# Kernel optimization log

Measured on AMD Instinct MI355X. Metric: run time of the kernel, lower is better.

Reference implementation:

```python
import jax, jax.numpy as jnp
import numpy as np

EMBED = 1024
HEADS = 16
HEAD_DIM = EMBED // HEADS


def setup_inputs() -> dict:
    key = jax.random.key(0)
    ks = jax.random.split(key, 7)
    B, Sd, Se = 4, 2048, 2048
    dec = jax.random.normal(ks[0], (B, Sd, EMBED), dtype=jnp.float32)
    enc = jax.random.normal(ks[1], (B, Se, EMBED), dtype=jnp.float32)
    scale = 1.0 / np.sqrt(EMBED)
    W_q = jax.random.normal(ks[2], (EMBED, EMBED), dtype=jnp.float32) * scale
    W_k = jax.random.normal(ks[3], (EMBED, EMBED), dtype=jnp.float32) * scale
    W_v = jax.random.normal(ks[4], (EMBED, EMBED), dtype=jnp.float32) * scale
    W_o = jax.random.normal(ks[5], (EMBED, EMBED), dtype=jnp.float32) * scale
    b_o = jax.random.normal(ks[6], (EMBED,), dtype=jnp.float32) * 0.01
    return {"decoder_input": dec, "encoder_output": enc,
            "W_q": W_q, "W_k": W_k, "W_v": W_v, "W_o": W_o, "b_o": b_o}


def reference(decoder_input, encoder_output, W_q, W_k, W_v, W_o, b_o):
    B, Sd, E = decoder_input.shape
    Se = encoder_output.shape[1]
    # projections (nn.Linear applies x @ W.T; here W is stored as [in, out])
    Q = (decoder_input @ W_q).reshape(B, Sd, HEADS, HEAD_DIM)
    K = (encoder_output @ W_k).reshape(B, Se, HEADS, HEAD_DIM)
    V = (encoder_output @ W_v).reshape(B, Se, HEADS, HEAD_DIM)
    # scores: [B, H, Sd, Se]
    scores = jnp.einsum('bqhd,bkhd->bhqk', Q, K) / jnp.sqrt(jnp.float32(HEAD_DIM))
    attn = jax.nn.softmax(scores, axis=-1)
    out = jnp.einsum('bhqk,bkhd->bqhd', attn, V).reshape(B, Sd, E)
    return out @ W_o + b_o
```

## Files before the change

kernel.cpp:

```cpp
#include <hip/hip_runtime.h>
#include <hip/hip_bf16.h>

namespace {

typedef __attribute__((ext_vector_type(8))) short bf16x8;
typedef __attribute__((ext_vector_type(4))) float f32x4;
typedef __attribute__((ext_vector_type(4))) unsigned u32x4v;

constexpr int BATCH = 4;
constexpr int SEQ   = 2048;
constexpr int EMB   = 1024;
constexpr int NH    = 16;
constexpr int HD    = 64;
constexpr int MTOT  = BATCH * SEQ;
constexpr float LOG2E = 1.44269504088896f;
constexpr float SOFTMAX_C = 16.0f;

__device__ __forceinline__ unsigned short f2bf(float x) {
    unsigned int u = __float_as_uint(x);
    u += 0x7fffu + ((u >> 16) & 1u);
    return (unsigned short)(u >> 16);
}

__device__ __forceinline__ void gl_lds16(const void* g, void* l) {
    __builtin_amdgcn_global_load_lds(
        (const __attribute__((address_space(1))) unsigned int*)g,
        (__attribute__((address_space(3))) unsigned int*)l, 16, 0, 0);
}

__global__ __launch_bounds__(256)
void prep(const float* __restrict__ dec, const float* __restrict__ enc,
          unsigned short* __restrict__ decb, unsigned short* __restrict__ encb,
          const float* __restrict__ W0, const float* __restrict__ W1,
          const float* __restrict__ W2, const float* __restrict__ W3,
          unsigned short* __restrict__ WtBase, float qscale)
{
    __shared__ __align__(16) unsigned short Ts[64][65];
    const int tid = threadIdx.x;
    const int bid = blockIdx.x;
    if (bid < 16384) {
        const int zz = bid >> 13;
        const int i = (bid & 8191) * 256 + tid;
        const float* src = zz ? enc : dec;
        unsigned short* dst = zz ? encb : decb;
        float4 v = ((const float4*)src)[i];
        ushort4 o;
        o.x = f2bf(v.x); o.y = f2bf(v.y); o.z = f2bf(v.z); o.w = f2bf(v.w);
        ((ushort4*)dst)[i] = o;
        return;
    }
    const int zid = bid - 16384;
    const int z = zid >> 8;
    const float* W = (z == 0) ? W0 : (z == 1) ? W1 : (z == 2) ? W2 : W3;
    unsigned short* Wt = WtBase + (size_t)z * EMB * EMB;
    const float scale = (z == 0) ? qscale : 1.0f;
    const int n0 = (zid & 15) * 64, k0 = ((zid >> 4) & 15) * 64;
    #pragma unroll
    for (int i = 0; i < 4; ++i) {
        int id = tid + i * 256;
        int r = id >> 4, q = id & 15;
        float4 v = *(const float4*)&W[(size_t)(k0 + r) * EMB + n0 + q * 4];
        Ts[q * 4 + 0][r] = f2bf(v.x * scale);
        Ts[q * 4 + 1][r] = f2bf(v.y * scale);
        Ts[q * 4 + 2][r] = f2bf(v.z * scale);
        Ts[q * 4 + 3][r] = f2bf(v.w * scale);
    }
    __syncthreads();
    #pragma unroll
    for (int i = 0; i < 4; ++i) {
        int id = tid + i * 256;
        int rn = id >> 4, q = id & 15;
        ushort4 o;
        o.x = Ts[rn][q * 4 + 0]; o.y = Ts[rn][q * 4 + 1];
        o.z = Ts[rn][q * 4 + 2]; o.w = Ts[rn][q * 4 + 3];
        *(ushort4*)&Wt[(size_t)(n0 + rn) * EMB + k0 + q * 4] = o;
    }
}

enum OutKind { OUT_BF16R, OUT_F32B, OUT_VTK };

template<int OK>
__device__ __forceinline__
void gemm_body(unsigned short* lds,
               const unsigned short* __restrict__ A, const unsigned short* __restrict__ Bt,
               const float* __restrict__ bias, void* __restrict__ Cout,
               int m0, int n0, int N, int Kd)
{
    const int tid  = threadIdx.x;
    const int lane = tid & 63, wave = tid >> 6;
    const int g = lane >> 4, c = lane & 15;
    const int wm = (wave & 1) * 64, wn = (wave >> 1) * 64;

    const int r0 = tid >> 2, s = tid & 3;
    const int sg = s ^ ((r0 + (r0 >> 2)) & 3);
    const unsigned short* ga0 = A  + (size_t)(m0 + r0)      * Kd + sg * 8;
    const unsigned short* ga1 = A  + (size_t)(m0 + r0 + 64) * Kd + sg * 8;
    const unsigned short* gb0 = Bt + (size_t)(n0 + r0)      * Kd + sg * 8;
    const unsigned short* gb1 = Bt + (size_t)(n0 + r0 + 64) * Kd + sg * 8;
    const int lo0 = tid * 8, lo1 = (256 + tid) * 8;

    const int cs = (c + (c >> 2)) & 3;

    f32x4 acc[4][4];
    #pragma unroll
    for (int i = 0; i < 4; ++i)
        #pragma unroll
        for (int j = 0; j < 4; ++j) acc[i][j] = (f32x4)0.0f;

    gl_lds16(ga0, &lds[lo0]);        gl_lds16(ga1, &lds[lo1]);
    gl_lds16(gb0, &lds[8192 + lo0]); gl_lds16(gb1, &lds[8192 + lo1]);
    ga0 += 32; ga1 += 32; gb0 += 32; gb1 += 32;
    __syncthreads();

    const int KT = Kd / 32;
    for (int kt = 0; kt < KT; kt += 2) {
        #pragma unroll
        for (int h2 = 0; h2 < 2; ++h2) {
            const int k = kt + h2;
            const int bcur = h2 * 4096, bnxt = (h2 ^ 1) * 4096;
            if (k + 1 < KT) {
                gl_lds16(ga0, &lds[bnxt + lo0]);        gl_lds16(ga1, &lds[bnxt + lo1]);
                gl_lds16(gb0, &lds[8192 + bnxt + lo0]); gl_lds16(gb1, &lds[8192 + bnxt + lo1]);
                ga0 += 32; ga1 += 32; gb0 += 32; gb1 += 32;
            }
            bf16x8 af[4], bfr[4];
            #pragma unroll
            for (int mt = 0; mt < 4; ++mt)
                af[mt]  = *(const bf16x8*)&lds[bcur + (wm + mt * 16 + c) * 32 + (g ^ cs) * 8];
            #pragma unroll
            for (int nt = 0; nt < 4; ++nt)
                bfr[nt] = *(const bf16x8*)&lds[8192 + bcur + (wn + nt * 16 + c) * 32 + (g ^ cs) * 8];
            #pragma unroll
            for (int mt = 0; mt < 4; ++mt)
                #pragma unroll
                for (int nt = 0; nt < 4; ++nt) {
                    if (OK == OUT_VTK)
                        acc[mt][nt] = __builtin_amdgcn_mfma_f32_16x16x32_bf16(af[mt], bfr[nt], acc[mt][nt], 0, 0, 0);
                    else
                        acc[mt][nt] = __builtin_amdgcn_mfma_f32_16x16x32_bf16(bfr[nt], af[mt], acc[mt][nt], 0, 0, 0);
                }
            __syncthreads();
        }
    }

    if (OK == OUT_VTK) {
        unsigned short* Vt = (unsigned short*)Cout;
        #pragma unroll
        for (int mt = 0; mt < 4; ++mt) {
            int m  = m0 + wm + mt * 16 + 4 * g;
            int bb = m >> 11, sl = m & 2047;
            int sp = (sl & ~31) | (((sl >> 2) & 3) << 3) | (((sl >> 4) & 1) << 2);
            #pragma unroll
            for (int nt = 0; nt < 4; ++nt) {
                int np = n0 + wn + nt * 16 + c;
                ushort4 o;
                o.x = f2bf(acc[mt][nt][0]); o.y = f2bf(acc[mt][nt][1]);
                o.z = f2bf(acc[mt][nt][2]); o.w = f2bf(acc[mt][nt][3]);
                *(ushort4*)&Vt[((size_t)bb * 1024 + np) * SEQ + sp] = o;
            }
        }
        return;
    }

    if (OK == OUT_BF16R) {
        unsigned short* C = (unsigned short*)Cout;
        #pragma unroll
        for (int mt = 0; mt < 4; ++mt) {
            int m = m0 + wm + mt * 16 + c;
            #pragma unroll
            for (int nt = 0; nt < 4; ++nt) {
                int n = n0 + wn + nt * 16 + 4 * g;
                unsigned u0, u1;
                asm("v_cvt_pk_bf16_f32 %0, %1, %2" : "=v"(u0) : "v"(acc[mt][nt][0]), "v"(acc[mt][nt][1]));
                asm("v_cvt_pk_bf16_f32 %0, %1, %2" : "=v"(u1) : "v"(acc[mt][nt][2]), "v"(acc[mt][nt][3]));
                uint2 st; st.x = u0; st.y = u1;
                *(uint2*)&C[(size_t)m * N + n] = st;
            }
        }
        return;
    }

    {
        float* C = (float*)Cout;
        #pragma unroll
        for (int nt = 0; nt < 4; ++nt) {
            int n = n0 + wn + nt * 16 + 4 * g;
            float4 bv = *(const float4*)&bias[n];
            #pragma unroll
            for (int mt = 0; mt < 4; ++mt) {
                int m = m0 + wm + mt * 16 + c;
                float4 o;
                o.x = acc[mt][nt][0] + bv.x;
                o.y = acc[mt][nt][1] + bv.y;
                o.z = acc[mt][nt][2] + bv.z;
                o.w = acc[mt][nt][3] + bv.w;
                *(float4*)&C[(size_t)m * N + n] = o;
            }
        }
    }
}

__global__ __launch_bounds__(256)
void proj_fused(const unsigned short* __restrict__ decb, const unsigned short* __restrict__ encb,
                const unsigned short* __restrict__ WtBase,
                unsigned short* __restrict__ Qb, unsigned short* __restrict__ Kb,
                unsigned short* __restrict__ Vtg)
{
    __shared__ __align__(16) unsigned short lds[16384];
    const int fid = blockIdx.y * 24 + blockIdx.x;
    const int xcd = fid & 7, idx = fid >> 3;
    const int mt  = (xcd << 3) | (idx / 24);
    const int nt  = idx % 24;
    const int m0  = mt * 128;
    const size_t SML = (size_t)EMB * EMB;
    if (nt < 8) {
        gemm_body<OUT_BF16R>(lds, decb, WtBase, nullptr, Qb, m0, nt * 128, EMB, EMB);
    } else if (nt < 16) {
        gemm_body<OUT_BF16R>(lds, encb, WtBase + SML, nullptr, Kb,
                             m0, (nt - 8) * 128, EMB, EMB);
    } else {
        gemm_body<OUT_VTK>(lds, encb, WtBase + 2 * SML, nullptr, Vtg,
                           m0, (nt - 16) * 128, 0, EMB);
    }
}

__global__ __launch_bounds__(256)
void proj_out(const unsigned short* __restrict__ Ob, const unsigned short* __restrict__ WoT,
              const float* __restrict__ bo, float* __restrict__ out)
{
    __shared__ __align__(16) unsigned short lds[16384];
    const int fid = blockIdx.y * 8 + blockIdx.x;
    const int xcd = fid & 7, idx = fid >> 3;
    const int mt  = (xcd << 3) | (idx >> 3);
    const int nt  = idx & 7;
    gemm_body<OUT_F32B>(lds, Ob, WoT, bo, out, mt * 128, nt * 128, EMB, EMB);
}

__global__ __launch_bounds__(256)
void attn(const unsigned short* __restrict__ Q, const unsigned short* __restrict__ K,
          const unsigned short* __restrict__ Vt, unsigned short* __restrict__ O)
{
    __shared__ __align__(16) unsigned short Ks[2][64 * 64];
    __shared__ __align__(16) unsigned short Vs[2][64 * 64];

    const int tid  = threadIdx.x;
    const int lane = tid & 63, wave = tid >> 6;
    const int g = lane >> 4, c = lane & 15, c7 = c & 7;

    const int fid  = blockIdx.y * 32 + blockIdx.x;
    const int xcd  = fid & 7, idx = fid >> 3;
    const int bh   = (xcd << 3) | (idx >> 5);
    const int qblk = idx & 31;
    const int b = bh >> 4, h = bh & 15;
    const int qw = qblk * 64 + wave * 16;

    const unsigned short* Qp0 = Q + (size_t)(b * SEQ + qw + c) * EMB + h * HD;
    bf16x8 qb[2];
    qb[0] = *(const bf16x8*)(Qp0 + g * 8);
    qb[1] = *(const bf16x8*)(Qp0 + 32 + g * 8);

    const int r0 = tid >> 3, s8 = tid & 7;
    const int sg = s8 ^ (r0 & 7);
    const unsigned short* gK0 = K + ((size_t)b * SEQ + r0) * EMB + h * HD + sg * 8;
    const unsigned short* gK1 = gK0 + (size_t)32 * EMB;
    const unsigned short* gV0 = Vt + (size_t)bh * HD * SEQ + (size_t)r0 * SEQ + sg * 8;
    const unsigned short* gV1 = gV0 + (size_t)32 * SEQ;
    const int lo0 = tid * 8, lo1 = (256 + tid) * 8;

    f32x4 oac[4];
    #pragma unroll
    for (int dt = 0; dt < 4; ++dt) oac[dt] = (f32x4)0.0f;
    f32x4 lacc = (f32x4)0.0f;
    const f32x4 minit = {-SOFTMAX_C, -SOFTMAX_C, -SOFTMAX_C, -SOFTMAX_C};
    const short onebf = (short)0x3F80;
    const bf16x8 vones = {onebf, onebf, onebf, onebf, onebf, onebf, onebf, onebf};

    gl_lds16(gK0, &Ks[0][lo0]); gl_lds16(gK1, &Ks[0][lo1]);
    gl_lds16(gV0, &Vs[0][lo0]); gl_lds16(gV1, &Vs[0][lo1]);
    gK0 += (size_t)64 * EMB; gK1 += (size_t)64 * EMB; gV0 += 64; gV1 += 64;
    __syncthreads();

    constexpr int T = SEQ / 64;
    for (int t = 0; t < T; t += 2) {
        #pragma unroll
        for (int h2 = 0; h2 < 2; ++h2) {
            const int tt = t + h2;
            if (tt + 1 < T) {
                gl_lds16(gK0, &Ks[h2 ^ 1][lo0]); gl_lds16(gK1, &Ks[h2 ^ 1][lo1]);
                gl_lds16(gV0, &Vs[h2 ^ 1][lo0]); gl_lds16(gV1, &Vs[h2 ^ 1][lo1]);
                gK0 += (size_t)64 * EMB; gK1 += (size_t)64 * EMB;
                gV0 += 64;               gV1 += 64;
            }

            f32x4 st[4];
            __builtin_amdgcn_s_setprio(1);
            #pragma unroll
            for (int kt = 0; kt < 4; ++kt) {
                bf16x8 ka0 = *(const bf16x8*)&Ks[h2][(kt * 16 + c) * 64 + (g ^ c7) * 8];
                bf16x8 ka1 = *(const bf16x8*)&Ks[h2][(kt * 16 + c) * 64 + ((4 + g) ^ c7) * 8];
                st[kt] = __builtin_amdgcn_mfma_f32_16x16x32_bf16(ka0, qb[0], minit, 0, 0, 0);
                st[kt] = __builtin_amdgcn_mfma_f32_16x16x32_bf16(ka1, qb[1], st[kt], 0, 0, 0);
            }
            __builtin_amdgcn_s_setprio(0);

            bf16x8 pa[2];
            {
                unsigned uu[8];
                #pragma unroll
                for (int kt = 0; kt < 4; ++kt) {
                    float p0 = __builtin_amdgcn_exp2f(st[kt][0]);
                    float p1 = __builtin_amdgcn_exp2f(st[kt][1]);
                    float p2 = __builtin_amdgcn_exp2f(st[kt][2]);
                    float p3 = __builtin_amdgcn_exp2f(st[kt][3]);
                    asm("v_cvt_pk_bf16_f32 %0, %1, %2" : "=v"(uu[2 * kt])     : "v"(p0), "v"(p1));
                    asm("v_cvt_pk_bf16_f32 %0, %1, %2" : "=v"(uu[2 * kt + 1]) : "v"(p2), "v"(p3));
                }
                u32x4v w0 = {uu[0], uu[1], uu[2], uu[3]};
                u32x4v w1 = {uu[4], uu[5], uu[6], uu[7]};
                pa[0] = __builtin_bit_cast(bf16x8, w0);
                pa[1] = __builtin_bit_cast(bf16x8, w1);
            }

            __builtin_amdgcn_s_setprio(1);
            #pragma unroll
            for (int dt = 0; dt < 4; ++dt) {
                bf16x8 vb0 = *(const bf16x8*)&Vs[h2][(dt * 16 + c) * 64 + (g ^ c7) * 8];
                bf16x8 vb1 = *(const bf16x8*)&Vs[h2][(dt * 16 + c) * 64 + ((4 + g) ^ c7) * 8];
                oac[dt] = __builtin_amdgcn_mfma_f32_16x16x32_bf16(pa[0], vb0, oac[dt], 0, 0, 0);
                oac[dt] = __builtin_amdgcn_mfma_f32_16x16x32_bf16(pa[1], vb1, oac[dt], 0, 0, 0);
            }
            lacc = __builtin_amdgcn_mfma_f32_16x16x32_bf16(pa[0], vones, lacc, 0, 0, 0);
            lacc = __builtin_amdgcn_mfma_f32_16x16x32_bf16(pa[1], vones, lacc, 0, 0, 0);
            __builtin_amdgcn_s_setprio(0);

            __syncthreads();
        }
    }

    unsigned short* Op = O + (size_t)(b * SEQ + qw) * EMB + h * HD;
    #pragma unroll
    for (int r = 0; r < 4; ++r) {
        float linv = 1.0f / lacc[r];
        #pragma unroll
        for (int dt = 0; dt < 4; ++dt)
            Op[(size_t)(4 * g + r) * EMB + dt * 16 + c] = f2bf(oac[dt][r] * linv);
    }
}

}

extern "C" void kernel_launch(void* const* d_in, const int* in_sizes, int n_in,
                              void* d_out, int out_size, void* d_ws, size_t ws_size,
                              hipStream_t stream)
{
    const float* dec = (const float*)d_in[0];
    const float* enc = (const float*)d_in[1];
    const float* Wq  = (const float*)d_in[2];
    const float* Wk  = (const float*)d_in[3];
    const float* Wv  = (const float*)d_in[4];
    const float* Wo  = (const float*)d_in[5];
    const float* bo  = (const float*)d_in[6];
    float* out = (float*)d_out;

    const size_t BIG = (size_t)MTOT * EMB;
    const size_t SML = (size_t)EMB * EMB;
    unsigned short* decb = (unsigned short*)d_ws;
    unsigned short* encb = decb + BIG;
    unsigned short* WqT  = encb + BIG;
    unsigned short* WoT  = WqT + 3 * SML;
    unsigned short* Qb   = WqT + 4 * SML;
    unsigned short* Kb   = Qb + BIG;
    unsigned short* Vtg  = Kb + BIG;
    unsigned short* Ob   = Vtg + BIG;

    dim3 blk(256);

    prep<<<dim3(16384 + 1024), blk, 0, stream>>>(
        dec, enc, decb, encb, Wq, Wk, Wv, Wo, WqT, 0.125f * LOG2E);

    proj_fused<<<dim3(24, MTOT / 128), blk, 0, stream>>>(decb, encb, WqT, Qb, Kb, Vtg);

    attn<<<dim3(SEQ / 64, BATCH * NH), blk, 0, stream>>>(Qb, Kb, Vtg, Ob);

    proj_out<<<dim3(EMB / 128, MTOT / 128), blk, 0, stream>>>(Ob, WoT, bo, out);
}
```

Baseline: 302.3 us.

## Halve attention KV tile to raise occupancy and reorder GEMM tile mapping

The attention kernel now streams K/V in 32-key tiles instead of 64, which halves LDS use, and requests 8 blocks per CU through launch bounds so more waves can hide latency. Each iteration therefore does half the MFMA work, with twice as many barriers and loop trips. The projection GEMMs also change their block-to-tile mapping so that consecutive blocks on an XCD share the N tile (weights) across M tiles, aiming at better L2 reuse. Risks are the extra synchronization overhead per key and possible register pressure from the occupancy bound.

Measured after the change: 325.7 us. 7.8% more time.

```diff
diff --git a/kernel.cpp b/kernel.cpp
--- a/kernel.cpp
+++ b/kernel.cpp
@@ -209,8 +209,8 @@
     __shared__ __align__(16) unsigned short lds[16384];
     const int fid = blockIdx.y * 24 + blockIdx.x;
     const int xcd = fid & 7, idx = fid >> 3;
-    const int mt  = (xcd << 3) | (idx / 24);
-    const int nt  = idx % 24;
+    const int nt  = idx >> 3;
+    const int mt  = (xcd << 3) | (idx & 7);
     const int m0  = mt * 128;
     const size_t SML = (size_t)EMB * EMB;
     if (nt < 8) {
@@ -231,21 +231,21 @@
     __shared__ __align__(16) unsigned short lds[16384];
     const int fid = blockIdx.y * 8 + blockIdx.x;
     const int xcd = fid & 7, idx = fid >> 3;
-    const int mt  = (xcd << 3) | (idx >> 3);
-    const int nt  = idx & 7;
+    const int nt  = idx >> 3;
+    const int mt  = (xcd << 3) | (idx & 7);
     gemm_body<OUT_F32B>(lds, Ob, WoT, bo, out, mt * 128, nt * 128, EMB, EMB);
 }
 
-__global__ __launch_bounds__(256)
+__global__ __launch_bounds__(256, 8)
 void attn(const unsigned short* __restrict__ Q, const unsigned short* __restrict__ K,
           const unsigned short* __restrict__ Vt, unsigned short* __restrict__ O)
 {
-    __shared__ __align__(16) unsigned short Ks[2][64 * 64];
-    __shared__ __align__(16) unsigned short Vs[2][64 * 64];
+    __shared__ __align__(16) unsigned short Ks[2][32 * 64];
+    __shared__ __align__(16) unsigned short Vs[2][64 * 32];
 
     const int tid  = threadIdx.x;
     const int lane = tid & 63, wave = tid >> 6;
-    const int g = lane >> 4, c = lane & 15, c7 = c & 7;
+    const int g = lane >> 4, c = lane & 15, c7 = c & 7, c3 = c & 3;
 
     const int fid  = blockIdx.y * 32 + blockIdx.x;
     const int xcd  = fid & 7, idx = fid >> 3;
@@ -259,13 +259,13 @@
     qb[0] = *(const bf16x8*)(Qp0 + g * 8);
     qb[1] = *(const bf16x8*)(Qp0 + 32 + g * 8);
 
-    const int r0 = tid >> 3, s8 = tid & 7;
-    const int sg = s8 ^ (r0 & 7);
-    const unsigned short* gK0 = K + ((size_t)b * SEQ + r0) * EMB + h * HD + sg * 8;
-    const unsigned short* gK1 = gK0 + (size_t)32 * EMB;
-    const unsigned short* gV0 = Vt + (size_t)bh * HD * SEQ + (size_t)r0 * SEQ + sg * 8;
-    const unsigned short* gV1 = gV0 + (size_t)32 * SEQ;
-    const int lo0 = tid * 8, lo1 = (256 + tid) * 8;
+    const int r0k = tid >> 3, s8 = tid & 7;
+    const int sgk = s8 ^ (r0k & 7);
+    const unsigned short* gK = K + ((size_t)b * SEQ + r0k) * EMB + h * HD + sgk * 8;
+    const int r0v = tid >> 2, s4 = tid & 3;
+    const int sgv = s4 ^ (r0v & 3);
+    const unsigned short* gV = Vt + ((size_t)bh * HD + r0v) * SEQ + sgv * 8;
+    const int lo = tid * 8;
 
     f32x4 oac[4];
     #pragma unroll
@@ -275,27 +275,24 @@
     const short onebf = (short)0x3F80;
     const bf16x8 vones = {onebf, onebf, onebf, onebf, onebf, onebf, onebf, onebf};
 
-    gl_lds16(gK0, &Ks[0][lo0]); gl_lds16(gK1, &Ks[0][lo1]);
-    gl_lds16(gV0, &Vs[0][lo0]); gl_lds16(gV1, &Vs[0][lo1]);
-    gK0 += (size_t)64 * EMB; gK1 += (size_t)64 * EMB; gV0 += 64; gV1 += 64;
+    gl_lds16(gK, &Ks[0][lo]); gl_lds16(gV, &Vs[0][lo]);
+    gK += (size_t)32 * EMB; gV += 32;
     __syncthreads();
 
-    constexpr int T = SEQ / 64;
+    constexpr int T = SEQ / 32;
     for (int t = 0; t < T; t += 2) {
         #pragma unroll
         for (int h2 = 0; h2 < 2; ++h2) {
             const int tt = t + h2;
             if (tt + 1 < T) {
-                gl_lds16(gK0, &Ks[h2 ^ 1][lo0]); gl_lds16(gK1, &Ks[h2 ^ 1][lo1]);
-                gl_lds16(gV0, &Vs[h2 ^ 1][lo0]); gl_lds16(gV1, &Vs[h2 ^ 1][lo1]);
-                gK0 += (size_t)64 * EMB; gK1 += (size_t)64 * EMB;
-                gV0 += 64;               gV1 += 64;
-            }
-
-            f32x4 st[4];
+                gl_lds16(gK, &Ks[h2 ^ 1][lo]); gl_lds16(gV, &Vs[h2 ^ 1][lo]);
+                gK += (size_t)32 * EMB; gV += 32;
+            }
+
+            f32x4 st[2];
             __builtin_amdgcn_s_setprio(1);
             #pragma unroll
-            for (int kt = 0; kt < 4; ++kt) {
+            for (int kt = 0; kt < 2; ++kt) {
                 bf16x8 ka0 = *(const bf16x8*)&Ks[h2][(kt * 16 + c) * 64 + (g ^ c7) * 8];
                 bf16x8 ka1 = *(const bf16x8*)&Ks[h2][(kt * 16 + c) * 64 + ((4 + g) ^ c7) * 8];
                 st[kt] = __builtin_amdgcn_mfma_f32_16x16x32_bf16(ka0, qb[0], minit, 0, 0, 0);
@@ -303,11 +300,11 @@
             }
             __builtin_amdgcn_s_setprio(0);
 
-            bf16x8 pa[2];
+            bf16x8 pa;
             {
-                unsigned uu[8];
+                unsigned uu[4];
                 #pragma unroll
-                for (int kt = 0; kt < 4; ++kt) {
+                for (int kt = 0; kt < 2; ++kt) {
                     float p0 = __builtin_amdgcn_exp2f(st[kt][0]);
                     float p1 = __builtin_amdgcn_exp2f(st[kt][1]);
                     float p2 = __builtin_amdgcn_exp2f(st[kt][2]);
@@ -315,22 +312,17 @@
                     asm("v_cvt_pk_bf16_f32 %0, %1, %2" : "=v"(uu[2 * kt])     : "v"(p0), "v"(p1));
                     asm("v_cvt_pk_bf16_f32 %0, %1, %2" : "=v"(uu[2 * kt + 1]) : "v"(p2), "v"(p3));
                 }
-                u32x4v w0 = {uu[0], uu[1], uu[2], uu[3]};
-                u32x4v w1 = {uu[4], uu[5], uu[6], uu[7]};
-                pa[0] = __builtin_bit_cast(bf16x8, w0);
-                pa[1] = __builtin_bit_cast(bf16x8, w1);
+                u32x4v w = {uu[0], uu[1], uu[2], uu[3]};
+                pa = __builtin_bit_cast(bf16x8, w);
             }
 
             __builtin_amdgcn_s_setprio(1);
             #pragma unroll
             for (int dt = 0; dt < 4; ++dt) {
-                bf16x8 vb0 = *(const bf16x8*)&Vs[h2][(dt * 16 + c) * 64 + (g ^ c7) * 8];
-                bf16x8 vb1 = *(const bf16x8*)&Vs[h2][(dt * 16 + c) * 64 + ((4 + g) ^ c7) * 8];
-                oac[dt] = __builtin_amdgcn_mfma_f32_16x16x32_bf16(pa[0], vb0, oac[dt], 0, 0, 0);
-                oac[dt] = __builtin_amdgcn_mfma_f32_16x16x32_bf16(pa[1], vb1, oac[dt], 0, 0, 0);
-            }
-            lacc = __builtin_amdgcn_mfma_f32_16x16x32_bf16(pa[0], vones, lacc, 0, 0, 0);
-            lacc = __builtin_amdgcn_mfma_f32_16x16x32_bf16(pa[1], vones, lacc, 0, 0, 0);
+                bf16x8 vb = *(const bf16x8*)&Vs[h2][(dt * 16 + c) * 32 + (g ^ c3) * 8];
+                oac[dt] = __builtin_amdgcn_mfma_f32_16x16x32_bf16(pa, vb, oac[dt], 0, 0, 0);
+            }
+            lacc = __builtin_amdgcn_mfma_f32_16x16x32_bf16(pa, vones, lacc, 0, 0, 0);
             __builtin_amdgcn_s_setprio(0);
 
             __syncthreads();
```
